# Kernel optimization log

Measured on AMD Instinct MI355X. Metric: run time of the kernel, lower is better.

Reference implementation:

```python
import jax, jax.numpy as jnp
import numpy as np

DIM = 1024
NUM_HEADS = 16
HEAD_DIM = DIM // NUM_HEADS


def setup_inputs() -> dict:
    key = jax.random.key(0)
    k1, k2, k3, k4, k5 = jax.random.split(key, 5)
    s = 0.02
    return {
        "x": jax.random.normal(k1, (2, 2048, DIM), dtype=jnp.float32),
        "Wq": jax.random.normal(k2, (DIM, DIM), dtype=jnp.float32) * s,
        "Wk": jax.random.normal(k3, (DIM, DIM), dtype=jnp.float32) * s,
        "Wv": jax.random.normal(k4, (DIM, DIM), dtype=jnp.float32) * s,
        "Wo": jax.random.normal(k5, (DIM, DIM), dtype=jnp.float32) * s,
    }


def rotate_half(x):
    x1, x2 = x[..., : x.shape[-1] // 2], x[..., x.shape[-1] // 2 :]
    return jnp.concatenate([-x2, x1], axis=-1)


def rope_cos_sin(seq_len, head_dim, dtype):
    inv_freq = 1.0 / (10000.0 ** (jnp.arange(0, head_dim, 2, dtype=jnp.float32) / head_dim))
    t = jnp.arange(seq_len, dtype=jnp.float32)
    freqs = jnp.einsum("i,j->ij", t, inv_freq)  # [S, head_dim/2]
    emb = jnp.concatenate([freqs, freqs], axis=-1)  # [S, head_dim]
    return jnp.cos(emb).astype(dtype), jnp.sin(emb).astype(dtype)


def reference(x, Wq, Wk, Wv, Wo):
    B, S, D = x.shape
    H, Hd = NUM_HEADS, HEAD_DIM
    scale = Hd ** -0.5

    def proj(W):
        # nn.Linear: x @ W.T; reshape to [B, H, S, Hd]
        return (x @ W.T).reshape(B, S, H, Hd).transpose(0, 2, 1, 3)

    q, k, v = proj(Wq), proj(Wk), proj(Wv)
    cos, sin = rope_cos_sin(S, Hd, x.dtype)  # [S, Hd], broadcast over B,H
    q = q * cos + rotate_half(q) * sin
    k = k * cos + rotate_half(k) * sin

    attn = jnp.einsum("bhqd,bhkd->bhqk", q, k) * scale  # [B,H,S,S]
    causal = jnp.triu(jnp.ones((S, S), dtype=bool), k=1)
    attn = jnp.where(causal, -jnp.inf, attn)
    attn = jax.nn.softmax(attn, axis=-1)
    out = jnp.einsum("bhqk,bhkd->bhqd", attn, v)
    out = out.transpose(0, 2, 1, 3).reshape(B, S, D)
    return out @ Wo.T
```

## Files before the change

### kernel.cpp

```cpp
#include <hip/hip_runtime.h>

#define DIM 1024
#define NHEADS 16
#define HD 64
#define SEQ 2048
#define BATCH 2
#define MROWS (BATCH*SEQ)
#define QKVLD 3072

typedef _Float16 h16;
typedef __attribute__((ext_vector_type(2))) _Float16 h16x2;
typedef __attribute__((ext_vector_type(2))) __fp16 fp16x2;
typedef __attribute__((ext_vector_type(4))) _Float16 h16x4;
typedef __attribute__((ext_vector_type(8))) _Float16 h16x8;
typedef __attribute__((ext_vector_type(4))) float f32x4;
typedef __attribute__((ext_vector_type(16))) float f32x16;

union U2 { fp16x2 g; h16x2 h; unsigned u; };

__global__ __launch_bounds__(256) void prep_k(
    const float* __restrict__ x,  const float* __restrict__ wq,
    const float* __restrict__ wk, const float* __restrict__ wv,
    const float* __restrict__ wo,
    h16* __restrict__ xh, h16* __restrict__ wqkvh, h16* __restrict__ woh,
    float2* __restrict__ rope)
{
    const int NX = MROWS * DIM / 4;
    const int NW = DIM * DIM / 4;
    int gid = blockIdx.x * 256 + threadIdx.x;
    if (gid < NX) {
        float4 v = *reinterpret_cast<const float4*>(x + (size_t)gid * 4);
        h16x4 o; o.x=(h16)v.x; o.y=(h16)v.y; o.z=(h16)v.z; o.w=(h16)v.w;
        *reinterpret_cast<h16x4*>(xh + (size_t)gid * 4) = o;
    } else if (gid < NX + 3 * NW) {
        int j = gid - NX;
        int w = j >> 18, e = j & (NW - 1);
        const float* s = (w == 0) ? wq : (w == 1) ? wk : wv;
        float4 v = *reinterpret_cast<const float4*>(s + (size_t)e * 4);
        h16x4 o; o.x=(h16)v.x; o.y=(h16)v.y; o.z=(h16)v.z; o.w=(h16)v.w;
        *reinterpret_cast<h16x4*>(wqkvh + (size_t)w * DIM * DIM + (size_t)e * 4) = o;
    } else if (gid < NX + 4 * NW) {
        int e = gid - NX - 3 * NW;
        float4 v = *reinterpret_cast<const float4*>(wo + (size_t)e * 4);
        h16x4 o; o.x=(h16)v.x; o.y=(h16)v.y; o.z=(h16)v.z; o.w=(h16)v.w;
        *reinterpret_cast<h16x4*>(woh + (size_t)e * 4) = o;
    } else {
        int t = gid - NX - 4 * NW;
        int s = t >> 5, j = t & 31;
        float inv = powf(10000.0f, -(float)j / 32.0f);
        float ang = (float)s * inv;
        rope[t] = make_float2(cosf(ang), sinf(ang));
    }
}

template<int MODE>
__global__ __launch_bounds__(256) void gemm_bt(
    const h16* __restrict__ A, const h16* __restrict__ Bw,
    void* __restrict__ Cout, const float2* __restrict__ rope,
    int M, int N, int K)
{
    __shared__ h16 As[128][64];
    __shared__ h16 Bs[128][64];
    const int tid  = threadIdx.x;
    const int wave = tid >> 6, lane = tid & 63;
    const int lr = lane & 15, lg = lane >> 4;
    const int wm = wave >> 1, wn = wave & 1;
    const int ntn = N >> 7;
    const int bm = blockIdx.x / ntn, bn = blockIdx.x % ntn;
    const int m0 = bm << 7, n0 = bn << 7;

    f32x4 acc[4][4];
#pragma unroll
    for (int i = 0; i < 4; ++i)
#pragma unroll
        for (int j = 0; j < 4; ++j) acc[i][j] = (f32x4){0.f, 0.f, 0.f, 0.f};

    const int arow = lane >> 3;
    const int acol = (lane & 7) << 3;

    for (int k0 = 0; k0 < K; k0 += 64) {
#pragma unroll
        for (int q = 0; q < 4; ++q) {
            int ch = wave * 4 + q;
            const h16* ga = A + (size_t)(m0 + ch * 8 + arow) * K + k0 + acol;
            __builtin_amdgcn_global_load_lds(
                (const __attribute__((address_space(1))) void*)ga,
                (__attribute__((address_space(3))) void*)(&As[ch * 8][0]), 16, 0, 0);
            const h16* gb = Bw + (size_t)(n0 + ch * 8 + arow) * K + k0 + acol;
            __builtin_amdgcn_global_load_lds(
                (const __attribute__((address_space(1))) void*)gb,
                (__attribute__((address_space(3))) void*)(&Bs[ch * 8][0]), 16, 0, 0);
        }
        __syncthreads();
#pragma unroll
        for (int ks = 0; ks < 2; ++ks) {
            h16x8 af[4], bf[4];
#pragma unroll
            for (int mi = 0; mi < 4; ++mi)
                af[mi] = *(const h16x8*)&As[wm * 64 + mi * 16 + lr][ks * 32 + lg * 8];
#pragma unroll
            for (int ni = 0; ni < 4; ++ni)
                bf[ni] = *(const h16x8*)&Bs[wn * 64 + ni * 16 + lr][ks * 32 + lg * 8];
#pragma unroll
            for (int mi = 0; mi < 4; ++mi)
#pragma unroll
                for (int ni = 0; ni < 4; ++ni)
                    acc[mi][ni] = __builtin_amdgcn_mfma_f32_16x16x32_f16(
                        af[mi], bf[ni], acc[mi][ni], 0, 0, 0);
        }
        __syncthreads();
    }

    if (MODE == 2) {
        float* C = (float*)Cout;
#pragma unroll
        for (int mi = 0; mi < 4; ++mi)
#pragma unroll
            for (int i = 0; i < 4; ++i) {
                int row = m0 + wm * 64 + mi * 16 + lg * 4 + i;
#pragma unroll
                for (int ni = 0; ni < 4; ++ni) {
                    int col = n0 + wn * 64 + ni * 16 + lr;
                    C[(size_t)row * N + col] = acc[mi][ni][i];
                }
            }
    } else {
        h16* C = (h16*)Cout;
        const int region = n0 >> 10;
        if (region == 2) {
#pragma unroll
            for (int mi = 0; mi < 4; ++mi)
#pragma unroll
                for (int i = 0; i < 4; ++i) {
                    int row = m0 + wm * 64 + mi * 16 + lg * 4 + i;
#pragma unroll
                    for (int ni = 0; ni < 4; ++ni) {
                        int col = n0 + wn * 64 + ni * 16 + lr;
                        C[(size_t)row * N + col] = (h16)acc[mi][ni][i];
                    }
                }
        } else {
#pragma unroll
            for (int mi = 0; mi < 4; ++mi)
#pragma unroll
                for (int i = 0; i < 4; ++i) {
                    int row = m0 + wm * 64 + mi * 16 + lg * 4 + i;
                    int s = row & (SEQ - 1);
#pragma unroll
                    for (int ni = 0; ni < 4; ++ni) {
                        int col = n0 + wn * 64 + ni * 16 + lr;
                        int d = col & 63;
                        float2 cs = rope[(s << 5) + (d & 31)];
                        float v  = acc[mi][ni][i];
                        float vp = acc[mi][ni ^ 2][i];
                        float rh = (d < 32) ? -vp : vp;
                        C[(size_t)row * N + col] = (h16)(v * cs.x + rh * cs.y);
                    }
                }
        }
    }
}

__global__ __launch_bounds__(256) void attn_k(
    const h16* __restrict__ QKV, h16* __restrict__ O)
{
    __shared__ h16 Ks[2][64][64];
    __shared__ h16 Vt[2][64][72];

    const int bx = blockIdx.x, by = blockIdx.y;
    const int b = by >> 4, h = by & 15;
    const int qt = b ? bx : (15 - bx);
    const int tid = threadIdx.x, wave = tid >> 6, lane = tid & 63;
    const int lq = lane & 31, hi = lane >> 5;

    const h16* Qb = QKV + (size_t)b * SEQ * QKVLD + h * HD;
    const h16* Kb = Qb + DIM;
    const h16* Vb = Qb + 2 * DIM;

    const int qw0 = qt * 128 + wave * 32;

    h16x8 qf[4];
    {
        const h16* qp = Qb + (size_t)(qw0 + lq) * QKVLD + 8 * hi;
        const h16 qs = (h16)(0.125f * 1.44269504f);
#pragma unroll
        for (int kb = 0; kb < 4; ++kb) {
            qf[kb] = *(const h16x8*)(qp + 16 * kb);
            qf[kb] *= qs;
        }
    }

    float l_run = 0.f;
    f32x16 accd[2];
#pragma unroll
    for (int i = 0; i < 16; ++i) { accd[0][i] = 0.f; accd[1][i] = 0.f; }

    const int kr = tid >> 3, kc = tid & 7;
    h16x8 vv0, vv1;

#define STAGE_K(bufi, kv0_) do {                                                   \
    const h16* gk0_ = Kb + (size_t)((kv0_) + kr) * QKVLD + ((kc ^ (kr & 7)) << 3); \
    __builtin_amdgcn_global_load_lds(                                              \
        (const __attribute__((address_space(1))) void*)gk0_,                       \
        (__attribute__((address_space(3))) void*)(&Ks[bufi][wave * 8][0]), 16, 0, 0); \
    const h16* gk1_ = Kb + (size_t)((kv0_) + 32 + kr) * QKVLD + ((kc ^ (kr & 7)) << 3); \
    __builtin_amdgcn_global_load_lds(                                              \
        (const __attribute__((address_space(1))) void*)gk1_,                       \
        (__attribute__((address_space(3))) void*)(&Ks[bufi][32 + wave * 8][0]), 16, 0, 0); \
} while (0)

#define VLOAD(kv0_) do {                                                           \
    const h16* gv_ = Vb + (size_t)((kv0_) + lane) * QKVLD + 16 * wave;             \
    vv0 = *(const h16x8*)gv_; vv1 = *(const h16x8*)(gv_ + 8);                      \
} while (0)

#define VWRITE(bufi) do {                                                          \
    _Pragma("unroll")                                                              \
    for (int j_ = 0; j_ < 8; ++j_) {                                               \
        Vt[bufi][16 * wave + j_][lane] = vv0[j_];                                  \
        Vt[bufi][16 * wave + 8 + j_][lane] = vv1[j_];                              \
    }                                                                              \
} while (0)

    const int nkv = 2 * qt + 2;
    STAGE_K(0, 0); VLOAD(0); VWRITE(0);
    __syncthreads();

    for (int t = 0; t < nkv; ++t) {
        const int cur = t & 1;
        const int kv0 = t << 6;
        const bool pf = (t + 1 < nkv);
        if (pf) { STAGE_K(cur ^ 1, kv0 + 64); VLOAD(kv0 + 64); }

        const bool act = (kv0 <= qw0 + 31);
        float p[32];
        if (act) {
            f32x16 s0, s1;
#pragma unroll
            for (int i = 0; i < 16; ++i) { s0[i] = 0.f; s1[i] = 0.f; }
            const int sk = lq & 7;
            __builtin_amdgcn_s_setprio(1);
#pragma unroll
            for (int kb = 0; kb < 4; ++kb) {
                const int ch = ((2 * kb + hi) ^ sk) << 3;
                h16x8 kf0 = *(const h16x8*)&Ks[cur][lq][ch];
                h16x8 kf1 = *(const h16x8*)&Ks[cur][32 + lq][ch];
                s0 = __builtin_amdgcn_mfma_f32_32x32x16_f16(kf0, qf[kb], s0, 0, 0, 0);
                s1 = __builtin_amdgcn_mfma_f32_32x32x16_f16(kf1, qf[kb], s1, 0, 0, 0);
            }
            __builtin_amdgcn_s_setprio(0);
            const bool full = (kv0 + 64 <= qw0);
            float ls = 0.f;
            if (full) {
#pragma unroll
                for (int r = 0; r < 16; ++r) {
                    p[r]      = exp2f(s0[r]);
                    p[16 + r] = exp2f(s1[r]);
                    ls += p[r] + p[16 + r];
                }
            } else {
                const int Lq = qw0 + lq - kv0;
#pragma unroll
                for (int r = 0; r < 16; ++r) {
                    const int kvl = (r & 3) + 8 * (r >> 2) + 4 * hi;
                    float e0 = exp2f(s0[r]);
                    float e1 = exp2f(s1[r]);
                    p[r]      = (kvl <= Lq)      ? e0 : 0.f;
                    p[16 + r] = (kvl + 32 <= Lq) ? e1 : 0.f;
                    ls += p[r] + p[16 + r];
                }
            }
            l_run += ls;
        }
        if (pf) VWRITE(cur ^ 1);
        if (act) {
            h16x8 pfrag[4];
#pragma unroll
            for (int kva = 0; kva < 2; ++kva) {
                const int o = 16 * kva;
                U2 x, y, z, w, x2, y2, z2, w2;
                x.g  = __builtin_amdgcn_cvt_pkrtz(p[o+0],  p[o+1]);
                y.g  = __builtin_amdgcn_cvt_pkrtz(p[o+2],  p[o+3]);
                z.g  = __builtin_amdgcn_cvt_pkrtz(p[o+4],  p[o+5]);
                w.g  = __builtin_amdgcn_cvt_pkrtz(p[o+6],  p[o+7]);
                x2.g = __builtin_amdgcn_cvt_pkrtz(p[o+8],  p[o+9]);
                y2.g = __builtin_amdgcn_cvt_pkrtz(p[o+10], p[o+11]);
                z2.g = __builtin_amdgcn_cvt_pkrtz(p[o+12], p[o+13]);
                w2.g = __builtin_amdgcn_cvt_pkrtz(p[o+14], p[o+15]);
                asm volatile("v_permlane32_swap_b32 %0, %1" : "+v"(x.u),  "+v"(z.u));
                asm volatile("v_permlane32_swap_b32 %0, %1" : "+v"(y.u),  "+v"(w.u));
                asm volatile("v_permlane32_swap_b32 %0, %1" : "+v"(x2.u), "+v"(z2.u));
                asm volatile("v_permlane32_swap_b32 %0, %1" : "+v"(y2.u), "+v"(w2.u));
                h16x8 f0, f1;
                f0[0]=x.h.x;  f0[1]=x.h.y;  f0[2]=y.h.x;  f0[3]=y.h.y;
                f0[4]=z.h.x;  f0[5]=z.h.y;  f0[6]=w.h.x;  f0[7]=w.h.y;
                f1[0]=x2.h.x; f1[1]=x2.h.y; f1[2]=y2.h.x; f1[3]=y2.h.y;
                f1[4]=z2.h.x; f1[5]=z2.h.y; f1[6]=w2.h.x; f1[7]=w2.h.y;
                pfrag[2*kva]   = f0;
                pfrag[2*kva+1] = f1;
            }
            __builtin_amdgcn_s_setprio(1);
#pragma unroll
            for (int da = 0; da < 2; ++da)
#pragma unroll
                for (int kvb = 0; kvb < 4; ++kvb) {
                    h16x8 vf = *(const h16x8*)&Vt[cur][32 * da + lq][16 * kvb + 8 * hi];
                    accd[da] = __builtin_amdgcn_mfma_f32_32x32x16_f16(vf, pfrag[kvb], accd[da], 0, 0, 0);
                }
            __builtin_amdgcn_s_setprio(0);
        }
        __syncthreads();
    }

    float lt = l_run + __shfl_xor(l_run, 32);
    float inv = 1.0f / lt;
    h16* Ob = O + (size_t)b * SEQ * DIM + h * HD + (size_t)(qw0 + lq) * DIM;
#pragma unroll
    for (int da = 0; da < 2; ++da)
#pragma unroll
        for (int r = 0; r < 16; r += 2) {
            int d = 32 * da + (r & 3) + 8 * (r >> 2) + 4 * hi;
            h16x2 ov;
            ov.x = (h16)(accd[da][r] * inv);
            ov.y = (h16)(accd[da][r + 1] * inv);
            *(h16x2*)(Ob + d) = ov;
        }
#undef STAGE_K
#undef VLOAD
#undef VWRITE
}

extern "C" void kernel_launch(void* const* d_in, const int* in_sizes, int n_in,
                              void* d_out, int out_size, void* d_ws, size_t ws_size,
                              hipStream_t stream)
{
    const float* x  = (const float*)d_in[0];
    const float* Wq = (const float*)d_in[1];
    const float* Wk = (const float*)d_in[2];
    const float* Wv = (const float*)d_in[3];
    const float* Wo = (const float*)d_in[4];

    char* ws = (char*)d_ws;
    h16* xh     = (h16*)(ws);
    h16* wqkvh  = (h16*)(ws + ((size_t)8  << 20));
    h16* woh    = (h16*)(ws + ((size_t)14 << 20));
    h16* QKVd   = (h16*)(ws + ((size_t)16 << 20));
    h16* Od     = (h16*)(ws + ((size_t)40 << 20));
    float2* rope = (float2*)(ws + ((size_t)48 << 20));

    const int NX = MROWS * DIM / 4, NW = DIM * DIM / 4;
    prep_k<<<(NX + 4 * NW + SEQ * 32) / 256, 256, 0, stream>>>(
        x, Wq, Wk, Wv, Wo, xh, wqkvh, woh, rope);

    gemm_bt<1><<<(MROWS / 128) * (QKVLD / 128), 256, 0, stream>>>(
        xh, wqkvh, QKVd, rope, MROWS, QKVLD, DIM);

    attn_k<<<dim3(16, BATCH * NHEADS), 256, 0, stream>>>(QKVd, Od);

    gemm_bt<2><<<(MROWS / 128) * (DIM / 128), 256, 0, stream>>>(
        Od, woh, d_out, rope, MROWS, DIM, DIM);
}
```

Baseline: 144.9 us.

## Double-buffer GEMM LDS tiles and swizzle block order across XCDs

The projection GEMM now keeps two LDS buffers per operand, so the direct-to-LDS loads for the next K tile are issued before the MFMAs on the current tile. The aim is to hide global load latency behind compute and drop one barrier per iteration. Block IDs are also remapped in groups of eight, so that neighbouring output tiles land on the same XCD and share L2 reuse of A and B. The cost is twice the LDS per block (64 KB), which may reduce occupancy. The remap also assumes the grid size is divisible by 8.

New measurement: 145.8 us. Within noise of the previous version (+0.7%).

```diff
diff --git a/kernel.cpp b/kernel.cpp
--- a/kernel.cpp
+++ b/kernel.cpp
@@ -59,14 +59,17 @@
     void* __restrict__ Cout, const float2* __restrict__ rope,
     int M, int N, int K)
 {
-    __shared__ h16 As[128][64];
-    __shared__ h16 Bs[128][64];
+    __shared__ h16 As[2][128][64];
+    __shared__ h16 Bs[2][128][64];
     const int tid  = threadIdx.x;
     const int wave = tid >> 6, lane = tid & 63;
     const int lr = lane & 15, lg = lane >> 4;
     const int wm = wave >> 1, wn = wave & 1;
     const int ntn = N >> 7;
-    const int bm = blockIdx.x / ntn, bn = blockIdx.x % ntn;
+    const int cpx = gridDim.x >> 3;
+    const int bid = blockIdx.x;
+    const int swz = (bid & 7) * cpx + (bid >> 3);
+    const int bm = swz / ntn, bn = swz % ntn;
     const int m0 = bm << 7, n0 = bn << 7;
 
     f32x4 acc[4][4];
@@ -78,29 +81,36 @@
     const int arow = lane >> 3;
     const int acol = (lane & 7) << 3;
 
-    for (int k0 = 0; k0 < K; k0 += 64) {
-#pragma unroll
-        for (int q = 0; q < 4; ++q) {
-            int ch = wave * 4 + q;
-            const h16* ga = A + (size_t)(m0 + ch * 8 + arow) * K + k0 + acol;
-            __builtin_amdgcn_global_load_lds(
-                (const __attribute__((address_space(1))) void*)ga,
-                (__attribute__((address_space(3))) void*)(&As[ch * 8][0]), 16, 0, 0);
-            const h16* gb = Bw + (size_t)(n0 + ch * 8 + arow) * K + k0 + acol;
-            __builtin_amdgcn_global_load_lds(
-                (const __attribute__((address_space(1))) void*)gb,
-                (__attribute__((address_space(3))) void*)(&Bs[ch * 8][0]), 16, 0, 0);
-        }
-        __syncthreads();
+#define GSTAGE(buf, k0_) do {                                                      \
+    _Pragma("unroll")                                                              \
+    for (int q_ = 0; q_ < 4; ++q_) {                                               \
+        int ch_ = wave * 4 + q_;                                                   \
+        const h16* ga_ = A + (size_t)(m0 + ch_ * 8 + arow) * K + (k0_) + acol;     \
+        __builtin_amdgcn_global_load_lds(                                          \
+            (const __attribute__((address_space(1))) void*)ga_,                    \
+            (__attribute__((address_space(3))) void*)(&As[buf][ch_ * 8][0]), 16, 0, 0); \
+        const h16* gb_ = Bw + (size_t)(n0 + ch_ * 8 + arow) * K + (k0_) + acol;    \
+        __builtin_amdgcn_global_load_lds(                                          \
+            (const __attribute__((address_space(1))) void*)gb_,                    \
+            (__attribute__((address_space(3))) void*)(&Bs[buf][ch_ * 8][0]), 16, 0, 0); \
+    }                                                                              \
+} while (0)
+
+    const int NT = K >> 6;
+    GSTAGE(0, 0);
+    __syncthreads();
+    int cur = 0;
+    for (int t = 0; t < NT; ++t) {
+        if (t + 1 < NT) GSTAGE(cur ^ 1, (t + 1) << 6);
 #pragma unroll
         for (int ks = 0; ks < 2; ++ks) {
             h16x8 af[4], bf[4];
 #pragma unroll
             for (int mi = 0; mi < 4; ++mi)
-                af[mi] = *(const h16x8*)&As[wm * 64 + mi * 16 + lr][ks * 32 + lg * 8];
+                af[mi] = *(const h16x8*)&As[cur][wm * 64 + mi * 16 + lr][ks * 32 + lg * 8];
 #pragma unroll
             for (int ni = 0; ni < 4; ++ni)
-                bf[ni] = *(const h16x8*)&Bs[wn * 64 + ni * 16 + lr][ks * 32 + lg * 8];
+                bf[ni] = *(const h16x8*)&Bs[cur][wn * 64 + ni * 16 + lr][ks * 32 + lg * 8];
 #pragma unroll
             for (int mi = 0; mi < 4; ++mi)
 #pragma unroll
@@ -109,7 +119,9 @@
                         af[mi], bf[ni], acc[mi][ni], 0, 0, 0);
         }
         __syncthreads();
-    }
+        cur ^= 1;
+    }
+#undef GSTAGE
 
     if (MODE == 2) {
         float* C = (float*)Cout;
```

## Add 256x256 double-buffered QKV GEMM with direct global-to-LDS loads

Applied to the files above, without the earlier changes.

Replaces the 128x128 templated GEMM used for the QKV projection with a dedicated 512-thread kernel that computes 256x256 tiles. It double-buffers LDS, issues async global_load_lds copies with an XOR swizzle, and interleaves prefetch of the next K tile with MFMA work using s_setprio and explicit waitcnt and barriers. The output projection keeps the old 128x128 kernel, now specialised. The larger tile improves operand reuse, but the 128 KB of LDS and heavy register use may limit occupancy, and the grid of 16x12=192 blocks is small compared with the CU count.

After: 147.0 us. No clear change (+1.5%).

```diff
diff --git a/kernel.cpp b/kernel.cpp
--- a/kernel.cpp
+++ b/kernel.cpp
@@ -17,6 +17,9 @@
 typedef __attribute__((ext_vector_type(16))) float f32x16;
 
 union U2 { fp16x2 g; h16x2 h; unsigned u; };
+
+#define CBAR() do { asm volatile("" ::: "memory"); __builtin_amdgcn_s_barrier(); \
+                    asm volatile("" ::: "memory"); } while (0)
 
 __global__ __launch_bounds__(256) void prep_k(
     const float* __restrict__ x,  const float* __restrict__ wq,
@@ -53,11 +56,140 @@
     }
 }
 
-template<int MODE>
-__global__ __launch_bounds__(256) void gemm_bt(
+__global__ __launch_bounds__(512, 2) void gemm256_qkv(
     const h16* __restrict__ A, const h16* __restrict__ Bw,
-    void* __restrict__ Cout, const float2* __restrict__ rope,
-    int M, int N, int K)
+    h16* __restrict__ C, const float2* __restrict__ rope)
+{
+    __shared__ h16 As[2][256][64];
+    __shared__ h16 Bs[2][256][64];
+    const int tid = threadIdx.x, wave = tid >> 6, lane = tid & 63;
+    const int lr = lane & 15, lg = lane >> 4;
+    const int wm = wave >> 2, wn = wave & 3;
+    const int ntn = QKVLD >> 8;
+    const int bm = blockIdx.x / ntn, bn = blockIdx.x % ntn;
+    const int m0 = bm << 8, n0 = bn << 8;
+
+    const int srl = lane >> 3;
+    const int sgc = ((lane & 7) ^ srl) << 3;
+
+#define STAGE_HALF(buf, k0_, h_) do {                                               \
+    _Pragma("unroll")                                                               \
+    for (int j_ = 0; j_ < 2; ++j_) {                                                \
+        int rl_ = ((h_) & 1) * 128 + (j_ * 8 + wave) * 8;                           \
+        if ((h_) < 2) {                                                             \
+            const h16* g_ = A + (size_t)(m0 + rl_ + srl) * DIM + (k0_) + sgc;       \
+            __builtin_amdgcn_global_load_lds(                                       \
+                (const __attribute__((address_space(1))) void*)g_,                  \
+                (__attribute__((address_space(3))) void*)(&As[buf][rl_][0]), 16, 0, 0); \
+        } else {                                                                    \
+            const h16* g_ = Bw + (size_t)(n0 + rl_ + srl) * DIM + (k0_) + sgc;      \
+            __builtin_amdgcn_global_load_lds(                                       \
+                (const __attribute__((address_space(1))) void*)g_,                  \
+                (__attribute__((address_space(3))) void*)(&Bs[buf][rl_][0]), 16, 0, 0); \
+        }                                                                           \
+    }                                                                               \
+} while (0)
+
+    f32x4 acc[8][4];
+#pragma unroll
+    for (int i = 0; i < 8; ++i)
+#pragma unroll
+        for (int j = 0; j < 4; ++j) acc[i][j] = (f32x4){0.f, 0.f, 0.f, 0.f};
+
+    const int NT = DIM >> 6;
+#pragma unroll
+    for (int h = 0; h < 4; ++h) STAGE_HALF(0, 0, h);
+
+    int cur = 0;
+    const int cp = (lg << 2);
+    const int rx = 0;
+    (void)rx;
+    for (int t = 0; t < NT; ++t) {
+        const int k0n = (t + 1) << 6;
+        const bool pf = (t + 1 < NT);
+        h16x8 bfr[4][2];
+#pragma unroll
+        for (int p = 0; p < 4; ++p) {
+            if (pf) STAGE_HALF(cur ^ 1, k0n, p);
+            if (p == 0) {
+                if (pf) asm volatile("s_waitcnt vmcnt(2)" ::: "memory");
+                else    asm volatile("s_waitcnt vmcnt(0)" ::: "memory");
+                CBAR();
+            }
+            h16x8 afr[2][2];
+#pragma unroll
+            for (int e = 0; e < 2; ++e)
+#pragma unroll
+                for (int ks = 0; ks < 2; ++ks) {
+                    int r = wm * 128 + (2 * p + e) * 16 + lr;
+                    int cpos = ((ks << 2) + lg) ^ (lr & 7);
+                    afr[e][ks] = *(const h16x8*)&As[cur][r][cpos << 3];
+                }
+            if (p == 0) {
+#pragma unroll
+                for (int ni = 0; ni < 4; ++ni)
+#pragma unroll
+                    for (int ks = 0; ks < 2; ++ks) {
+                        int r = wn * 64 + ni * 16 + lr;
+                        int cpos = ((ks << 2) + lg) ^ (lr & 7);
+                        bfr[ni][ks] = *(const h16x8*)&Bs[cur][r][cpos << 3];
+                    }
+            } else {
+                CBAR();
+            }
+            __builtin_amdgcn_s_setprio(1);
+#pragma unroll
+            for (int e = 0; e < 2; ++e)
+#pragma unroll
+                for (int ni = 0; ni < 4; ++ni)
+#pragma unroll
+                    for (int ks = 0; ks < 2; ++ks)
+                        acc[2 * p + e][ni] = __builtin_amdgcn_mfma_f32_16x16x32_f16(
+                            afr[e][ks], bfr[ni][ks], acc[2 * p + e][ni], 0, 0, 0);
+            __builtin_amdgcn_s_setprio(0);
+            CBAR();
+        }
+        cur ^= 1;
+    }
+#undef STAGE_HALF
+
+    const int region = n0 >> 10;
+    if (region == 2) {
+#pragma unroll
+        for (int mi = 0; mi < 8; ++mi)
+#pragma unroll
+            for (int i = 0; i < 4; ++i) {
+                int row = m0 + wm * 128 + mi * 16 + lg * 4 + i;
+#pragma unroll
+                for (int ni = 0; ni < 4; ++ni) {
+                    int col = n0 + wn * 64 + ni * 16 + lr;
+                    C[(size_t)row * QKVLD + col] = (h16)acc[mi][ni][i];
+                }
+            }
+    } else {
+#pragma unroll
+        for (int mi = 0; mi < 8; ++mi)
+#pragma unroll
+            for (int i = 0; i < 4; ++i) {
+                int row = m0 + wm * 128 + mi * 16 + lg * 4 + i;
+                int s = row & (SEQ - 1);
+#pragma unroll
+                for (int ni = 0; ni < 4; ++ni) {
+                    int col = n0 + wn * 64 + ni * 16 + lr;
+                    int d = col & 63;
+                    float2 cs = rope[(s << 5) + (d & 31)];
+                    float v  = acc[mi][ni][i];
+                    float vp = acc[mi][ni ^ 2][i];
+                    float rh = (d < 32) ? -vp : vp;
+                    C[(size_t)row * QKVLD + col] = (h16)(v * cs.x + rh * cs.y);
+                }
+            }
+    }
+}
+
+__global__ __launch_bounds__(256) void gemm_out(
+    const h16* __restrict__ A, const h16* __restrict__ Bw,
+    float* __restrict__ C, int M, int N, int K)
 {
     __shared__ h16 As[128][64];
     __shared__ h16 Bs[128][64];
@@ -111,54 +243,17 @@
         __syncthreads();
     }
 
-    if (MODE == 2) {
-        float* C = (float*)Cout;
-#pragma unroll
-        for (int mi = 0; mi < 4; ++mi)
-#pragma unroll
-            for (int i = 0; i < 4; ++i) {
-                int row = m0 + wm * 64 + mi * 16 + lg * 4 + i;
-#pragma unroll
-                for (int ni = 0; ni < 4; ++ni) {
-                    int col = n0 + wn * 64 + ni * 16 + lr;
-                    C[(size_t)row * N + col] = acc[mi][ni][i];
-                }
-            }
-    } else {
-        h16* C = (h16*)Cout;
-        const int region = n0 >> 10;
-        if (region == 2) {
-#pragma unroll
-            for (int mi = 0; mi < 4; ++mi)
-#pragma unroll
-                for (int i = 0; i < 4; ++i) {
-                    int row = m0 + wm * 64 + mi * 16 + lg * 4 + i;
-#pragma unroll
-                    for (int ni = 0; ni < 4; ++ni) {
-                        int col = n0 + wn * 64 + ni * 16 + lr;
-                        C[(size_t)row * N + col] = (h16)acc[mi][ni][i];
-                    }
-                }
-        } else {
-#pragma unroll
-            for (int mi = 0; mi < 4; ++mi)
-#pragma unroll
-                for (int i = 0; i < 4; ++i) {
-                    int row = m0 + wm * 64 + mi * 16 + lg * 4 + i;
-                    int s = row & (SEQ - 1);
-#pragma unroll
-                    for (int ni = 0; ni < 4; ++ni) {
-                        int col = n0 + wn * 64 + ni * 16 + lr;
-                        int d = col & 63;
-                        float2 cs = rope[(s << 5) + (d & 31)];
-                        float v  = acc[mi][ni][i];
-                        float vp = acc[mi][ni ^ 2][i];
-                        float rh = (d < 32) ? -vp : vp;
-                        C[(size_t)row * N + col] = (h16)(v * cs.x + rh * cs.y);
-                    }
-                }
-        }
-    }
+#pragma unroll
+    for (int mi = 0; mi < 4; ++mi)
+#pragma unroll
+        for (int i = 0; i < 4; ++i) {
+            int row = m0 + wm * 64 + mi * 16 + lg * 4 + i;
+#pragma unroll
+            for (int ni = 0; ni < 4; ++ni) {
+                int col = n0 + wn * 64 + ni * 16 + lr;
+                C[(size_t)row * N + col] = acc[mi][ni][i];
+            }
+        }
 }
 
 __global__ __launch_bounds__(256) void attn_k(
@@ -352,11 +447,11 @@
     prep_k<<<(NX + 4 * NW + SEQ * 32) / 256, 256, 0, stream>>>(
         x, Wq, Wk, Wv, Wo, xh, wqkvh, woh, rope);
 
-    gemm_bt<1><<<(MROWS / 128) * (QKVLD / 128), 256, 0, stream>>>(
-        xh, wqkvh, QKVd, rope, MROWS, QKVLD, DIM);
+    gemm256_qkv<<<(MROWS / 256) * (QKVLD / 256), 512, 0, stream>>>(
+        xh, wqkvh, QKVd, rope);
 
     attn_k<<<dim3(16, BATCH * NHEADS), 256, 0, stream>>>(QKVd, Od);
 
-    gemm_bt<2><<<(MROWS / 128) * (DIM / 128), 256, 0, stream>>>(
-        Od, woh, d_out, rope, MROWS, DIM, DIM);
+    gemm_out<<<(MROWS / 128) * (DIM / 128), 256, 0, stream>>>(
+        Od, woh, (float*)d_out, MROWS, DIM, DIM);
 }
```
